# Kernel optimization log

Hardware: AMD Instinct MI355X
Metric: run time of the kernel (lower is better)

Reference implementation:

```python
import jax, jax.numpy as jnp
import numpy as np

NUM_HEADS = 12
HEAD_DIM = 32
GP_NUM = 20


def setup_inputs() -> dict:
    key = jax.random.key(0)
    k1, k2, k3, k4 = jax.random.split(key, 4)
    B, H, W, C = 4, 32, 32, 384
    att = NUM_HEADS * HEAD_DIM  # == C (required by single group_mode)
    x = jax.random.normal(k1, (B, H, W, C), dtype=jnp.float32)
    W_qkv = jax.random.normal(k2, (3 * att, C), dtype=jnp.float32) * (C ** -0.5)
    W_proj = jax.random.normal(k3, (C, att), dtype=jnp.float32) * (att ** -0.5)
    W_gp = jax.random.normal(k4, (GP_NUM, C), dtype=jnp.float32) * (C ** -0.5)
    return {"x": x, "W_qkv": W_qkv, "W_proj": W_proj, "W_gp": W_gp}


def reference(x, W_qkv, W_proj, W_gp):
    B, H, W_, C = x.shape
    N = H * W_
    h, d = NUM_HEADS, HEAD_DIM
    scale = d ** -0.5

    qkv = x.reshape(B, N, C) @ W_qkv.T                      # [B,N,3hd]
    q, k, v = jnp.split(qkv, 3, axis=-1)
    q = q.reshape(B, N, h, d).transpose(0, 2, 1, 3)          # [B,h,N,d]
    k = k.reshape(B, N, h, d).transpose(0, 2, 1, 3)
    v = v.reshape(B, N, h, d).transpose(0, 2, 1, 3)

    attn = jax.nn.softmax(jnp.einsum('bhnd,bhmd->bhnm', q, k) * scale, axis=-1)

    # single group mode: hard top-1 group assignment from all-head q
    q_all = q.transpose(0, 2, 1, 3).reshape(B, N, h * d)     # [B,N,hd]
    gw = q_all @ W_gp.T                                      # [B,N,GP_NUM]
    oh = jax.nn.one_hot(jnp.argmax(gw, axis=-1), GP_NUM, dtype=attn.dtype)
    G = jnp.einsum('bng,bmg->bnm', oh, oh)                   # [B,N,N] same-group mask
    Gh = jnp.concatenate([
        jnp.broadcast_to(G[:, None], (B, h // 2, N, N)),
        jnp.broadcast_to(1.0 - G[:, None], (B, h // 2, N, N)),
    ], axis=1)                                               # [B,h,N,N]

    attn = attn * Gh
    # unusual column-wise renorm: sum over query axis (dim=2)
    attn = attn / (attn.sum(axis=2, keepdims=True) + 1e-8)

    out = jnp.einsum('bhnm,bhmd->bhnd', attn, v)
    out = out.transpose(0, 2, 1, 3).reshape(B, H, W_, h * d)
    return out @ W_proj.T
```

## Files before the change

### kernel.cpp

```cpp
#include <hip/hip_runtime.h>
#include <hip/hip_bf16.h>


#define B_    4
#define N_    1024
#define C_    384
#define H3_   1152
#define NH_   12
#define HD_   32
#define GP_   20
#define BH_   48
#define SCALE 0.17677669529663687f

typedef __attribute__((ext_vector_type(8))) short bf16x8;
typedef __attribute__((ext_vector_type(4))) float f32x4;

static __device__ __forceinline__ unsigned short f2bf(float x) {
  union { float f; unsigned u; } v; v.f = x;
  unsigned r = v.u + 0x7fff + ((v.u >> 16) & 1);
  return (unsigned short)(r >> 16);
}
static __device__ __forceinline__ float bf2f(unsigned short h) {
  union { unsigned u; float f; } v; v.u = ((unsigned)h) << 16;
  return v.f;
}

__global__ __launch_bounds__(256) void conv3(const float* __restrict__ x,
                                             const float* __restrict__ wq,
                                             const float* __restrict__ wp,
                                             unsigned short* __restrict__ xh,
                                             unsigned short* __restrict__ xl,
                                             unsigned short* __restrict__ wqh,
                                             unsigned short* __restrict__ wql,
                                             unsigned short* __restrict__ wph,
                                             unsigned short* __restrict__ wpl) {
  const int NX = (4096 * C_) / 4, NQ = (H3_ * C_) / 4, NP = (C_ * C_) / 4;
  int idx = blockIdx.x * 256 + threadIdx.x;
  const float* src; unsigned short *dh, *dl; int o;
  if (idx < NX)            { src = x;  dh = xh;  dl = xl;  o = idx; }
  else if (idx < NX + NQ)  { src = wq; dh = wqh; dl = wql; o = idx - NX; }
  else if (idx < NX + NQ + NP) { src = wp; dh = wph; dl = wpl; o = idx - NX - NQ; }
  else return;
  float4 v = *(const float4*)(src + (size_t)o * 4);
  float a[4] = {v.x, v.y, v.z, v.w};
  unsigned short h[4], lo[4];
  #pragma unroll
  for (int i = 0; i < 4; ++i) { h[i] = f2bf(a[i]); lo[i] = f2bf(a[i] - bf2f(h[i])); }
  uint2 ph = {(unsigned)h[0]  | ((unsigned)h[1]  << 16),
              (unsigned)h[2]  | ((unsigned)h[3]  << 16)};
  uint2 pl = {(unsigned)lo[0] | ((unsigned)lo[1] << 16),
              (unsigned)lo[2] | ((unsigned)lo[3] << 16)};
  *(uint2*)(dh + (size_t)o * 4) = ph;
  *(uint2*)(dl + (size_t)o * 4) = pl;
}

__global__ __launch_bounds__(256) void wgp_fuse(const float* __restrict__ Wqkv,
                                                const float* __restrict__ Wgp,
                                                double* __restrict__ M) {
  int idx = blockIdx.x * 256 + threadIdx.x;
  if (idx >= GP_ * C_) return;
  int g = idx / C_, c = idx % C_;
  double acc = 0.0;
  for (int j = 0; j < C_; ++j)
    acc += (double)Wgp[g * C_ + j] * (double)Wqkv[(size_t)j * C_ + c];
  M[idx] = acc;
}

__global__ __launch_bounds__(320) void group_assign2(const float* __restrict__ x,
                                                     const double* __restrict__ M,
                                                     int* __restrict__ group) {
  __shared__ double sc[16][GP_];
  int tid = threadIdx.x;
  int r = tid / GP_, g = tid % GP_;
  int n = blockIdx.x * 16 + r;
  const float* row = x + (size_t)n * C_;
  const double* w = M + (size_t)g * C_;
  double acc = 0.0;
  for (int c = 0; c < C_; ++c) acc += (double)row[c] * w[c];
  sc[r][g] = acc;
  __syncthreads();
  if (g == 0) {
    int best = 0; double bv = sc[r][0];
    #pragma unroll
    for (int j = 1; j < GP_; ++j)
      if (sc[r][j] > bv) { bv = sc[r][j]; best = j; }
    group[n] = best;
  }
}

__global__ __launch_bounds__(256) void gemm_qkv(
    const unsigned short* __restrict__ Ah_g, const unsigned short* __restrict__ Al_g,
    const unsigned short* __restrict__ Bh_g, const unsigned short* __restrict__ Bl_g,
    unsigned short* __restrict__ Qh, unsigned short* __restrict__ Ql,
    unsigned short* __restrict__ Kh, unsigned short* __restrict__ Kl,
    float* __restrict__ Vf) {
  __shared__ __align__(16) unsigned short sAh[2][128 * 32];
  __shared__ __align__(16) unsigned short sAl[2][128 * 32];
  __shared__ __align__(16) unsigned short sBh[2][64 * 32];
  __shared__ __align__(16) unsigned short sBl[2][64 * 32];
  int tid = threadIdx.x;
  int l = tid & 63, w = tid >> 6;
  int lanelo = l & 15, g16 = l >> 4;
  int wr = w >> 1, wc = w & 1;
  int flat = blockIdx.x;
  int swz = (flat & 7) * 72 + (flat >> 3);
  int bm = swz / 18, bn = swz % 18;

  int ra = tid >> 2, c4 = tid & 3;
  const unsigned short* gAh0 = Ah_g + (size_t)(bm * 128 + ra) * C_ + c4 * 8;
  const unsigned short* gAl0 = Al_g + (size_t)(bm * 128 + ra) * C_ + c4 * 8;
  const unsigned short* gBh0 = Bh_g + (size_t)(bn * 64 + ra) * C_ + c4 * 8;
  const unsigned short* gBl0 = Bl_g + (size_t)(bn * 64 + ra) * C_ + c4 * 8;
  int dsa = ra * 32 + ((c4 ^ (ra & 3)) * 8);

  uint4 r0 = *(const uint4*)(gAh0);
  uint4 r1 = *(const uint4*)(gAh0 + (size_t)64 * C_);
  uint4 r2 = *(const uint4*)(gAl0);
  uint4 r3 = *(const uint4*)(gAl0 + (size_t)64 * C_);
  uint4 r4 = *(const uint4*)(gBh0);
  uint4 r5 = *(const uint4*)(gBl0);

  f32x4 acc[4][2];
  #pragma unroll
  for (int i = 0; i < 4; ++i)
    #pragma unroll
    for (int j = 0; j < 2; ++j) acc[i][j] = (f32x4){0.f, 0.f, 0.f, 0.f};

  int p = 0;
  for (int kk = 0; kk < 12; ++kk) {
    *(uint4*)(&sAh[p][dsa])           = r0;
    *(uint4*)(&sAh[p][dsa + 64 * 32]) = r1;
    *(uint4*)(&sAl[p][dsa])           = r2;
    *(uint4*)(&sAl[p][dsa + 64 * 32]) = r3;
    *(uint4*)(&sBh[p][dsa])           = r4;
    *(uint4*)(&sBl[p][dsa])           = r5;
    __syncthreads();
    if (kk < 11) {
      int ko = (kk + 1) * 32;
      r0 = *(const uint4*)(gAh0 + ko);
      r1 = *(const uint4*)(gAh0 + (size_t)64 * C_ + ko);
      r2 = *(const uint4*)(gAl0 + ko);
      r3 = *(const uint4*)(gAl0 + (size_t)64 * C_ + ko);
      r4 = *(const uint4*)(gBh0 + ko);
      r5 = *(const uint4*)(gBl0 + ko);
    }
    bf16x8 ah[4], al[4], bh8[2], bl8[2];
    #pragma unroll
    for (int i = 0; i < 4; ++i) {
      int row = wr * 64 + i * 16 + lanelo;
      int off = row * 32 + ((g16 ^ (row & 3)) * 8);
      ah[i] = *(const bf16x8*)(&sAh[p][off]);
      al[i] = *(const bf16x8*)(&sAl[p][off]);
    }
    #pragma unroll
    for (int j = 0; j < 2; ++j) {
      int row = wc * 32 + j * 16 + lanelo;
      int off = row * 32 + ((g16 ^ (row & 3)) * 8);
      bh8[j] = *(const bf16x8*)(&sBh[p][off]);
      bl8[j] = *(const bf16x8*)(&sBl[p][off]);
    }
    #pragma unroll
    for (int i = 0; i < 4; ++i)
      #pragma unroll
      for (int j = 0; j < 2; ++j) {
        acc[i][j] = __builtin_amdgcn_mfma_f32_16x16x32_bf16(ah[i], bh8[j], acc[i][j], 0, 0, 0);
        acc[i][j] = __builtin_amdgcn_mfma_f32_16x16x32_bf16(ah[i], bl8[j], acc[i][j], 0, 0, 0);
        acc[i][j] = __builtin_amdgcn_mfma_f32_16x16x32_bf16(al[i], bh8[j], acc[i][j], 0, 0, 0);
      }
    p ^= 1;
  }

  int region = bn / 6;
  #pragma unroll
  for (int i = 0; i < 4; ++i) {
    int mm0 = bm * 128 + wr * 64 + i * 16 + g16 * 4;
    #pragma unroll
    for (int j = 0; j < 2; ++j) {
      int c = bn * 64 + wc * 32 + j * 16 + lanelo;
      int cc = c - region * 384;
      #pragma unroll
      for (int t = 0; t < 4; ++t) {
        int mm = mm0 + t;
        int b = mm >> 10, n = mm & 1023;
        float v = acc[i][j][t];
        if (region == 0) {
          v *= SCALE;
          unsigned short h = f2bf(v), lo = f2bf(v - bf2f(h));
          size_t idx = ((size_t)(b * NH_ + (cc >> 5)) * N_ + n) * HD_ + (cc & 31);
          Qh[idx] = h; Ql[idx] = lo;
        } else if (region == 1) {
          unsigned short h = f2bf(v), lo = f2bf(v - bf2f(h));
          size_t idx = ((size_t)(b * NH_ + (cc >> 5)) * N_ + n) * HD_ + (cc & 31);
          Kh[idx] = h; Kl[idx] = lo;
        } else {
          Vf[(size_t)mm * C_ + cc] = v;
        }
      }
    }
  }
}

__global__ __launch_bounds__(256) void gemm_proj(
    const unsigned short* __restrict__ Ah_g, const unsigned short* __restrict__ Al_g,
    const unsigned short* __restrict__ Bh_g, const unsigned short* __restrict__ Bl_g,
    float* __restrict__ Cm) {
  __shared__ __align__(16) unsigned short sAh[2][64 * 32];
  __shared__ __align__(16) unsigned short sAl[2][64 * 32];
  __shared__ __align__(16) unsigned short sBh[2][64 * 32];
  __shared__ __align__(16) unsigned short sBl[2][64 * 32];
  int tid = threadIdx.x;
  int l = tid & 63, w = tid >> 6;
  int lanelo = l & 15, g16 = l >> 4;
  int wr = w >> 1, wc = w & 1;
  int flat = blockIdx.x;
  int swz = (flat & 7) * 48 + (flat >> 3);
  int bm = swz / 6, bn = swz % 6;

  int ra = tid >> 2, c4 = tid & 3;
  const unsigned short* gAh0 = Ah_g + (size_t)(bm * 64 + ra) * C_ + c4 * 8;
  const unsigned short* gAl0 = Al_g + (size_t)(bm * 64 + ra) * C_ + c4 * 8;
  const unsigned short* gBh0 = Bh_g + (size_t)(bn * 64 + ra) * C_ + c4 * 8;
  const unsigned short* gBl0 = Bl_g + (size_t)(bn * 64 + ra) * C_ + c4 * 8;
  int dsa = ra * 32 + ((c4 ^ (ra & 3)) * 8);

  uint4 r0 = *(const uint4*)(gAh0);
  uint4 r1 = *(const uint4*)(gAl0);
  uint4 r2 = *(const uint4*)(gBh0);
  uint4 r3 = *(const uint4*)(gBl0);

  f32x4 acc[2][2];
  #pragma unroll
  for (int i = 0; i < 2; ++i)
    #pragma unroll
    for (int j = 0; j < 2; ++j) acc[i][j] = (f32x4){0.f, 0.f, 0.f, 0.f};

  int p = 0;
  for (int kk = 0; kk < 12; ++kk) {
    *(uint4*)(&sAh[p][dsa]) = r0;
    *(uint4*)(&sAl[p][dsa]) = r1;
    *(uint4*)(&sBh[p][dsa]) = r2;
    *(uint4*)(&sBl[p][dsa]) = r3;
    __syncthreads();
    if (kk < 11) {
      int ko = (kk + 1) * 32;
      r0 = *(const uint4*)(gAh0 + ko);
      r1 = *(const uint4*)(gAl0 + ko);
      r2 = *(const uint4*)(gBh0 + ko);
      r3 = *(const uint4*)(gBl0 + ko);
    }
    bf16x8 ah[2], al[2], bh8[2], bl8[2];
    #pragma unroll
    for (int i = 0; i < 2; ++i) {
      int row = wr * 32 + i * 16 + lanelo;
      int off = row * 32 + ((g16 ^ (row & 3)) * 8);
      ah[i] = *(const bf16x8*)(&sAh[p][off]);
      al[i] = *(const bf16x8*)(&sAl[p][off]);
    }
    #pragma unroll
    for (int j = 0; j < 2; ++j) {
      int row = wc * 32 + j * 16 + lanelo;
      int off = row * 32 + ((g16 ^ (row & 3)) * 8);
      bh8[j] = *(const bf16x8*)(&sBh[p][off]);
      bl8[j] = *(const bf16x8*)(&sBl[p][off]);
    }
    #pragma unroll
    for (int i = 0; i < 2; ++i)
      #pragma unroll
      for (int j = 0; j < 2; ++j) {
        acc[i][j] = __builtin_amdgcn_mfma_f32_16x16x32_bf16(ah[i], bh8[j], acc[i][j], 0, 0, 0);
        acc[i][j] = __builtin_amdgcn_mfma_f32_16x16x32_bf16(ah[i], bl8[j], acc[i][j], 0, 0, 0);
        acc[i][j] = __builtin_amdgcn_mfma_f32_16x16x32_bf16(al[i], bh8[j], acc[i][j], 0, 0, 0);
      }
    p ^= 1;
  }
  #pragma unroll
  for (int i = 0; i < 2; ++i) {
    int mm = bm * 64 + wr * 32 + i * 16 + g16 * 4;
    #pragma unroll
    for (int j = 0; j < 2; ++j) {
      int c = bn * 64 + wc * 32 + j * 16 + lanelo;
      #pragma unroll
      for (int t = 0; t < 4; ++t)
        Cm[(size_t)(mm + t) * C_ + c] = acc[i][j][t];
    }
  }
}

__global__ __launch_bounds__(256) void score3(const unsigned short* __restrict__ Qh,
                                              const unsigned short* __restrict__ Ql,
                                              const unsigned short* __restrict__ Kh,
                                              const unsigned short* __restrict__ Kl,
                                              const int* __restrict__ group,
                                              float* __restrict__ rinv,
                                              float* __restrict__ colpart) {
  __shared__ __align__(16) unsigned short kbufh[4096];
  __shared__ __align__(16) unsigned short kbufl[4096];
  __shared__ float colpart_s[4][1024];
  __shared__ int g_s[1024];
  int tid = threadIdx.x;
  int l = tid & 63, w = tid >> 6;
  int lanelo = l & 15, g16 = l >> 4;
  int flat = blockIdx.y * 16 + blockIdx.x;
  int nf = (flat & 7) * 96 + (flat >> 3);
  int bh = nf >> 4, blk = nf & 15;
  int b = bh / NH_;
  bool samehead = ((bh % NH_) < NH_ / 2);
  int q0 = blk * 64 + w * 16;
  size_t bhb = (size_t)bh * (N_ * HD_);

  *(int4*)&g_s[tid * 4] = *(const int4*)(group + b * N_ + tid * 4);
  bf16x8 aQh = *(const bf16x8*)(Qh + bhb + (size_t)(q0 + lanelo) * HD_ + g16 * 8);
  bf16x8 aQl = *(const bf16x8*)(Ql + bhb + (size_t)(q0 + lanelo) * HD_ + g16 * 8);
  __syncthreads();
  int gq[4];
  #pragma unroll
  for (int t = 0; t < 4; ++t) gq[t] = g_s[q0 + g16 * 4 + t];

  float s4[4] = {0.f, 0.f, 0.f, 0.f};
  for (int ch = 0; ch < 8; ++ch) {
    __syncthreads();
    #pragma unroll
    for (int t2 = 0; t2 < 2; ++t2) {
      int f2 = t2 * 256 + tid;
      int row = f2 >> 2, c4 = f2 & 3;
      uint4 vh = *(const uint4*)(Kh + bhb + (size_t)(ch * 128 + row) * HD_ + c4 * 8);
      uint4 vl = *(const uint4*)(Kl + bhb + (size_t)(ch * 128 + row) * HD_ + c4 * 8);
      int phys = row * 64 + ((c4 ^ (row & 3)) << 4);
      *(uint4*)((char*)kbufh + phys) = vh;
      *(uint4*)((char*)kbufl + phys) = vl;
    }
    __syncthreads();
    #pragma unroll
    for (int kt2 = 0; kt2 < 8; ++kt2) {
      int kvl = kt2 * 16 + lanelo;
      int phys = kvl * 64 + ((g16 ^ (kvl & 3)) << 4);
      bf16x8 bh8 = *(const bf16x8*)((char*)kbufh + phys);
      bf16x8 bl8 = *(const bf16x8*)((char*)kbufl + phys);
      f32x4 acc = {0.f, 0.f, 0.f, 0.f};
      acc = __builtin_amdgcn_mfma_f32_16x16x32_bf16(aQh, bh8, acc, 0, 0, 0);
      acc = __builtin_amdgcn_mfma_f32_16x16x32_bf16(aQh, bl8, acc, 0, 0, 0);
      acc = __builtin_amdgcn_mfma_f32_16x16x32_bf16(aQl, bh8, acc, 0, 0, 0);
      #pragma unroll
      for (int t = 0; t < 4; ++t) s4[t] += __expf(acc[t]);
    }
  }
  float ri[4];
  #pragma unroll
  for (int t = 0; t < 4; ++t) {
    #pragma unroll
    for (int off = 1; off < 16; off <<= 1) s4[t] += __shfl_xor(s4[t], off);
    ri[t] = 1.0f / s4[t];
  }
  if (lanelo == 0) {
    #pragma unroll
    for (int t = 0; t < 4; ++t)
      rinv[(size_t)bh * N_ + q0 + g16 * 4 + t] = ri[t];
  }

  for (int ch = 0; ch < 8; ++ch) {
    __syncthreads();
    #pragma unroll
    for (int t2 = 0; t2 < 2; ++t2) {
      int f2 = t2 * 256 + tid;
      int row = f2 >> 2, c4 = f2 & 3;
      uint4 vh = *(const uint4*)(Kh + bhb + (size_t)(ch * 128 + row) * HD_ + c4 * 8);
      uint4 vl = *(const uint4*)(Kl + bhb + (size_t)(ch * 128 + row) * HD_ + c4 * 8);
      int phys = row * 64 + ((c4 ^ (row & 3)) << 4);
      *(uint4*)((char*)kbufh + phys) = vh;
      *(uint4*)((char*)kbufl + phys) = vl;
    }
    __syncthreads();
    #pragma unroll
    for (int kt2 = 0; kt2 < 8; ++kt2) {
      int kt = ch * 8 + kt2;
      int kvl = kt2 * 16 + lanelo;
      int phys = kvl * 64 + ((g16 ^ (kvl & 3)) << 4);
      bf16x8 bh8 = *(const bf16x8*)((char*)kbufh + phys);
      bf16x8 bl8 = *(const bf16x8*)((char*)kbufl + phys);
      f32x4 acc = {0.f, 0.f, 0.f, 0.f};
      acc = __builtin_amdgcn_mfma_f32_16x16x32_bf16(aQh, bh8, acc, 0, 0, 0);
      acc = __builtin_amdgcn_mfma_f32_16x16x32_bf16(aQh, bl8, acc, 0, 0, 0);
      acc = __builtin_amdgcn_mfma_f32_16x16x32_bf16(aQl, bh8, acc, 0, 0, 0);
      int gcol = g_s[kt * 16 + lanelo];
      float cs = 0.f;
      #pragma unroll
      for (int t = 0; t < 4; ++t) {
        bool keep = ((gcol == gq[t]) == samehead);
        cs += keep ? __expf(acc[t]) * ri[t] : 0.f;
      }
      cs += __shfl_xor(cs, 16);
      cs += __shfl_xor(cs, 32);
      if (l < 16) colpart_s[w][kt * 16 + l] = cs;
    }
  }
  __syncthreads();
  int c0 = tid * 4;
  float4 p0 = *(float4*)&colpart_s[0][c0];
  float4 p1 = *(float4*)&colpart_s[1][c0];
  float4 p2 = *(float4*)&colpart_s[2][c0];
  float4 p3 = *(float4*)&colpart_s[3][c0];
  float4 rr = {p0.x + p1.x + p2.x + p3.x, p0.y + p1.y + p2.y + p3.y,
               p0.z + p1.z + p2.z + p3.z, p0.w + p1.w + p2.w + p3.w};
  *(float4*)(colpart + ((size_t)(bh * 16 + blk)) * 1024 + c0) = rr;
}

__global__ __launch_bounds__(256) void vsplit(const float* __restrict__ colpart,
                                              const float* __restrict__ Vf,
                                              unsigned short* __restrict__ Vth,
                                              unsigned short* __restrict__ Vtl) {
  __shared__ float red[256];
  __shared__ float colinv_s[16];
  __shared__ unsigned short vh_s[32][16];
  __shared__ unsigned short vl_s[32][16];
  int tid = threadIdx.x;
  int flat = blockIdx.y * 64 + blockIdx.x;
  int nf = (flat & 7) * 384 + (flat >> 3);
  int bh = nf >> 6, mt = nf & 63;
  int b = bh / NH_, hd = bh % NH_;

  int p = tid >> 4, m16 = tid & 15;
  red[tid] = colpart[((size_t)(bh * 16 + p)) * 1024 + mt * 16 + m16];
  __syncthreads();
  #pragma unroll
  for (int st = 128; st >= 16; st >>= 1) {
    if (tid < st) red[tid] += red[tid + st];
    __syncthreads();
  }
  if (tid < 16) colinv_s[tid] = 1.0f / (red[tid] + 1e-8f);
  __syncthreads();
  if (tid < 128) {
    int m = tid >> 3, d4 = (tid & 7) * 4;
    float4 v = *(const float4*)(Vf + ((size_t)(b * N_ + mt * 16 + m)) * C_ +
                                hd * HD_ + d4);
    float ci = colinv_s[m];
    float va[4] = {v.x * ci, v.y * ci, v.z * ci, v.w * ci};
    #pragma unroll
    for (int i = 0; i < 4; ++i) {
      unsigned short h = f2bf(va[i]);
      vh_s[d4 + i][m] = h;
      vl_s[d4 + i][m] = f2bf(va[i] - bf2f(h));
    }
  }
  __syncthreads();
  if (tid < 64) {
    int d = tid >> 1, m8 = (tid & 1) * 8;
    uint4 h = *(uint4*)&vh_s[d][m8];
    *(uint4*)(Vth + ((size_t)bh * HD_ + d) * N_ + mt * 16 + m8) = h;
  } else if (tid < 128) {
    int t2 = tid - 64;
    int d = t2 >> 1, m8 = (t2 & 1) * 8;
    uint4 lo = *(uint4*)&vl_s[d][m8];
    *(uint4*)(Vtl + ((size_t)bh * HD_ + d) * N_ + mt * 16 + m8) = lo;
  }
}

__global__ __launch_bounds__(256) void pv3(const unsigned short* __restrict__ Qh,
                                           const unsigned short* __restrict__ Ql,
                                           const unsigned short* __restrict__ Kh,
                                           const unsigned short* __restrict__ Kl,
                                           const unsigned short* __restrict__ Vth,
                                           const unsigned short* __restrict__ Vtl,
                                           const int* __restrict__ group,
                                           const float* __restrict__ rinv,
                                           unsigned short* __restrict__ aoh,
                                           unsigned short* __restrict__ aol) {
  __shared__ __align__(16) unsigned short kbufh[4096];
  __shared__ __align__(16) unsigned short kbufl[4096];
  __shared__ __align__(16) unsigned short vbufh[4096];
  __shared__ __align__(16) unsigned short vbufl[4096];
  __shared__ __align__(16) float bounce[4][512];
  __shared__ int g_s[1024];
  int tid = threadIdx.x;
  int l = tid & 63, w = tid >> 6;
  int lanelo = l & 15, g16 = l >> 4;
  int flat = blockIdx.y * 16 + blockIdx.x;
  int nf = (flat & 7) * 96 + (flat >> 3);
  int bh = nf >> 4, blk = nf & 15;
  int b = bh / NH_, hd = bh % NH_;
  bool samehead = (hd < NH_ / 2);
  int q0 = blk * 64 + w * 16;
  size_t bhb = (size_t)bh * (N_ * HD_);

  *(int4*)&g_s[tid * 4] = *(const int4*)(group + b * N_ + tid * 4);
  bf16x8 aQh = *(const bf16x8*)(Qh + bhb + (size_t)(q0 + lanelo) * HD_ + g16 * 8);
  bf16x8 aQl = *(const bf16x8*)(Ql + bhb + (size_t)(q0 + lanelo) * HD_ + g16 * 8);
  float ri[4];
  #pragma unroll
  for (int t = 0; t < 4; ++t)
    ri[t] = rinv[(size_t)bh * N_ + q0 + g16 * 4 + t];
  __syncthreads();
  int gq[4];
  #pragma unroll
  for (int t = 0; t < 4; ++t) gq[t] = g_s[q0 + g16 * 4 + t];

  f32x4 o0 = {0.f, 0.f, 0.f, 0.f};
  f32x4 o1 = {0.f, 0.f, 0.f, 0.f};

  for (int ch = 0; ch < 8; ++ch) {
    __syncthreads();
    #pragma unroll
    for (int t2 = 0; t2 < 2; ++t2) {
      int f2 = t2 * 256 + tid;
      int row = f2 >> 2, c4 = f2 & 3;
      uint4 vh = *(const uint4*)(Kh + bhb + (size_t)(ch * 128 + row) * HD_ + c4 * 8);
      uint4 vl = *(const uint4*)(Kl + bhb + (size_t)(ch * 128 + row) * HD_ + c4 * 8);
      int phys = row * 64 + ((c4 ^ (row & 3)) << 4);
      *(uint4*)((char*)kbufh + phys) = vh;
      *(uint4*)((char*)kbufl + phys) = vl;
    }
    #pragma unroll
    for (int t2 = 0; t2 < 2; ++t2) {
      int f2 = t2 * 256 + tid;
      int d = f2 >> 4, c = f2 & 15;
      uint4 vh = *(const uint4*)(Vth + bhb + (size_t)d * N_ + ch * 128 + c * 8);
      uint4 vl = *(const uint4*)(Vtl + bhb + (size_t)d * N_ + ch * 128 + c * 8);
      int physc = c ^ (d & 15);
      *(uint4*)(vbufh + d * 128 + physc * 8) = vh;
      *(uint4*)(vbufl + d * 128 + physc * 8) = vl;
    }
    __syncthreads();

    #pragma unroll
    for (int pair = 0; pair < 4; ++pair) {
      f32x4 sa[2];
      #pragma unroll
      for (int half = 0; half < 2; ++half) {
        int kvl = pair * 32 + half * 16 + lanelo;
        int phys = kvl * 64 + ((g16 ^ (kvl & 3)) << 4);
        bf16x8 bh8 = *(const bf16x8*)((char*)kbufh + phys);
        bf16x8 bl8 = *(const bf16x8*)((char*)kbufl + phys);
        f32x4 acc = {0.f, 0.f, 0.f, 0.f};
        acc = __builtin_amdgcn_mfma_f32_16x16x32_bf16(aQh, bh8, acc, 0, 0, 0);
        acc = __builtin_amdgcn_mfma_f32_16x16x32_bf16(aQh, bl8, acc, 0, 0, 0);
        acc = __builtin_amdgcn_mfma_f32_16x16x32_bf16(aQl, bh8, acc, 0, 0, 0);
        sa[half] = acc;
      }
      #pragma unroll
      for (int half = 0; half < 2; ++half) {
        int kvloc = pair * 32 + half * 16 + lanelo;
        int gcol = g_s[ch * 128 + kvloc];
        int kv = half * 16 + lanelo;
        int chunk = kv >> 2;
        #pragma unroll
        for (int t = 0; t < 4; ++t) {
          bool keep = ((gcol == gq[t]) == samehead);
          float p = keep ? __expf(sa[half][t]) : 0.f;
          int q = g16 * 4 + t;
          bounce[w][q * 32 + ((chunk ^ (q & 7)) << 2) + (kv & 3)] = p;
        }
      }
      float pf[8];
      int q2 = lanelo;
      int c0i = (2 * g16) ^ (q2 & 7), c1i = (2 * g16 + 1) ^ (q2 & 7);
      *(float4*)&pf[0] = *(float4*)&bounce[w][q2 * 32 + c0i * 4];
      *(float4*)&pf[4] = *(float4*)&bounce[w][q2 * 32 + c1i * 4];
      bf16x8 pa;
      #pragma unroll
      for (int j = 0; j < 8; ++j) pa[j] = (short)f2bf(pf[j]);
      int vchunk = pair * 4 + g16;
      int d0 = lanelo, d1 = 16 + lanelo;
      bf16x8 v0h = *(const bf16x8*)(vbufh + d0 * 128 + ((vchunk ^ (d0 & 15)) << 3));
      bf16x8 v0l = *(const bf16x8*)(vbufl + d0 * 128 + ((vchunk ^ (d0 & 15)) << 3));
      bf16x8 v1h = *(const bf16x8*)(vbufh + d1 * 128 + ((vchunk ^ (d1 & 15)) << 3));
      bf16x8 v1l = *(const bf16x8*)(vbufl + d1 * 128 + ((vchunk ^ (d1 & 15)) << 3));
      o0 = __builtin_amdgcn_mfma_f32_16x16x32_bf16(pa, v0h, o0, 0, 0, 0);
      o0 = __builtin_amdgcn_mfma_f32_16x16x32_bf16(pa, v0l, o0, 0, 0, 0);
      o1 = __builtin_amdgcn_mfma_f32_16x16x32_bf16(pa, v1h, o1, 0, 0, 0);
      o1 = __builtin_amdgcn_mfma_f32_16x16x32_bf16(pa, v1l, o1, 0, 0, 0);
    }
  }
  #pragma unroll
  for (int t = 0; t < 4; ++t) {
    size_t row = (size_t)(b * N_ + q0 + g16 * 4 + t) * C_ + hd * HD_;
    float v0 = o0[t] * ri[t], v1 = o1[t] * ri[t];
    unsigned short h;
    h = f2bf(v0); aoh[row + lanelo]      = h; aol[row + lanelo]      = f2bf(v0 - bf2f(h));
    h = f2bf(v1); aoh[row + 16 + lanelo] = h; aol[row + 16 + lanelo] = f2bf(v1 - bf2f(h));
  }
}

extern "C" void kernel_launch(void* const* d_in, const int* in_sizes, int n_in,
                              void* d_out, int out_size, void* d_ws, size_t ws_size,
                              hipStream_t stream) {
  const float* x     = (const float*)d_in[0];
  const float* Wqkv  = (const float*)d_in[1];
  const float* Wproj = (const float*)d_in[2];
  const float* Wgp   = (const float*)d_in[3];
  float* out = (float*)d_out;

  char* base = (char*)d_ws;
  size_t off = 0;
  auto alloc = [&](size_t bytes) {
    void* p = base + off;
    off += (bytes + 255) & ~(size_t)255;
    return p;
  };
  float*  Vf      = (float*)alloc(4096ull * C_ * 4);
  float*  rinv    = (float*)alloc((size_t)BH_ * N_ * 4);
  float*  colpart = (float*)alloc((size_t)BH_ * 16 * N_ * 4);
  double* Mgp     = (double*)alloc((size_t)GP_ * C_ * 8);
  int*    group   = (int*)alloc(4096ull * 4);
  unsigned short* xh  = (unsigned short*)alloc(4096ull * C_ * 2);
  unsigned short* xl  = (unsigned short*)alloc(4096ull * C_ * 2);
  unsigned short* Wqh = (unsigned short*)alloc((size_t)H3_ * C_ * 2);
  unsigned short* Wql = (unsigned short*)alloc((size_t)H3_ * C_ * 2);
  unsigned short* Wph = (unsigned short*)alloc((size_t)C_ * C_ * 2);
  unsigned short* Wpl = (unsigned short*)alloc((size_t)C_ * C_ * 2);
  unsigned short* aoh = (unsigned short*)alloc(4096ull * C_ * 2);
  unsigned short* aol = (unsigned short*)alloc(4096ull * C_ * 2);
  const size_t BSZ = (size_t)BH_ * N_ * HD_;
  unsigned short* Qh  = (unsigned short*)alloc(BSZ * 2);
  unsigned short* Ql  = (unsigned short*)alloc(BSZ * 2);
  unsigned short* Kh  = (unsigned short*)alloc(BSZ * 2);
  unsigned short* Kl  = (unsigned short*)alloc(BSZ * 2);
  unsigned short* Vth = (unsigned short*)alloc(BSZ * 2);
  unsigned short* Vtl = (unsigned short*)alloc(BSZ * 2);

  conv3<<<dim3(2112), 256, 0, stream>>>(x, Wqkv, Wproj, xh, xl, Wqh, Wql, Wph, Wpl);
  wgp_fuse<<<dim3(30), 256, 0, stream>>>(Wqkv, Wgp, Mgp);
  group_assign2<<<dim3(256), 320, 0, stream>>>(x, Mgp, group);
  gemm_qkv<<<dim3(576), 256, 0, stream>>>(xh, xl, Wqh, Wql,
                                          Qh, Ql, Kh, Kl, Vf);
  score3<<<dim3(16, BH_), 256, 0, stream>>>(Qh, Ql, Kh, Kl, group, rinv, colpart);
  vsplit<<<dim3(64, BH_), 256, 0, stream>>>(colpart, Vf, Vth, Vtl);
  pv3<<<dim3(16, BH_), 256, 0, stream>>>(Qh, Ql, Kh, Kl, Vth, Vtl, group,
                                         rinv, aoh, aol);
  gemm_proj<<<dim3(384), 256, 0, stream>>>(aoh, aol, Wph, Wpl, out);
}
```

Measured before the change: 167.2 us.

## Materialize masked exp scores to global memory instead of recomputing QK in three passes

The score kernel now computes QK^T once. It writes the masked, unnormalized exp values as bf16 into a large global buffer E, tiled as 16 key columns by 1024 queries per block, and accumulates row sums in the same pass. This replaces the previous two-pass score kernel and the QK recomputation in the PV kernel. The Q scale now folds in log2(e) so exp2f can be used. A new colv kernel reduces the column sums from E weighted by rinv. pv5 reads E directly as the MFMA A operand, processes 128 queries per block, and prefetches V into registers. This trades repeated split-precision MFMA work for about 100 MB of extra global memory traffic and bf16 rounding of the probabilities.

```diff
diff --git a/kernel.cpp b/kernel.cpp
--- a/kernel.cpp
+++ b/kernel.cpp
@@ -10,7 +10,7 @@
 #define HD_   32
 #define GP_   20
 #define BH_   48
-#define SCALE 0.17677669529663687f
+#define QSCALE 0.2550029971791444f
 
 typedef __attribute__((ext_vector_type(8))) short bf16x8;
 typedef __attribute__((ext_vector_type(4))) float f32x4;
@@ -184,7 +184,7 @@
         int b = mm >> 10, n = mm & 1023;
         float v = acc[i][j][t];
         if (region == 0) {
-          v *= SCALE;
+          v *= QSCALE;
           unsigned short h = f2bf(v), lo = f2bf(v - bf2f(h));
           size_t idx = ((size_t)(b * NH_ + (cc >> 5)) * N_ + n) * HD_ + (cc & 31);
           Qh[idx] = h; Ql[idx] = lo;
@@ -286,16 +286,16 @@
   }
 }
 
-__global__ __launch_bounds__(256) void score3(const unsigned short* __restrict__ Qh,
+__global__ __launch_bounds__(256) void score5(const unsigned short* __restrict__ Qh,
                                               const unsigned short* __restrict__ Ql,
                                               const unsigned short* __restrict__ Kh,
                                               const unsigned short* __restrict__ Kl,
                                               const int* __restrict__ group,
                                               float* __restrict__ rinv,
-                                              float* __restrict__ colpart) {
+                                              unsigned short* __restrict__ E) {
   __shared__ __align__(16) unsigned short kbufh[4096];
   __shared__ __align__(16) unsigned short kbufl[4096];
-  __shared__ float colpart_s[4][1024];
+  __shared__ __align__(16) float bounce[4][256];
   __shared__ int g_s[1024];
   int tid = threadIdx.x;
   int l = tid & 63, w = tid >> 6;
@@ -317,45 +317,7 @@
   for (int t = 0; t < 4; ++t) gq[t] = g_s[q0 + g16 * 4 + t];
 
   float s4[4] = {0.f, 0.f, 0.f, 0.f};
-  for (int ch = 0; ch < 8; ++ch) {
-    __syncthreads();
-    #pragma unroll
-    for (int t2 = 0; t2 < 2; ++t2) {
-      int f2 = t2 * 256 + tid;
-      int row = f2 >> 2, c4 = f2 & 3;
-      uint4 vh = *(const uint4*)(Kh + bhb + (size_t)(ch * 128 + row) * HD_ + c4 * 8);
-      uint4 vl = *(const uint4*)(Kl + bhb + (size_t)(ch * 128 + row) * HD_ + c4 * 8);
-      int phys = row * 64 + ((c4 ^ (row & 3)) << 4);
-      *(uint4*)((char*)kbufh + phys) = vh;
-      *(uint4*)((char*)kbufl + phys) = vl;
-    }
-    __syncthreads();
-    #pragma unroll
-    for (int kt2 = 0; kt2 < 8; ++kt2) {
-      int kvl = kt2 * 16 + lanelo;
-      int phys = kvl * 64 + ((g16 ^ (kvl & 3)) << 4);
-      bf16x8 bh8 = *(const bf16x8*)((char*)kbufh + phys);
-      bf16x8 bl8 = *(const bf16x8*)((char*)kbufl + phys);
-      f32x4 acc = {0.f, 0.f, 0.f, 0.f};
-      acc = __builtin_amdgcn_mfma_f32_16x16x32_bf16(aQh, bh8, acc, 0, 0, 0);
-      acc = __builtin_amdgcn_mfma_f32_16x16x32_bf16(aQh, bl8, acc, 0, 0, 0);
-      acc = __builtin_amdgcn_mfma_f32_16x16x32_bf16(aQl, bh8, acc, 0, 0, 0);
-      #pragma unroll
-      for (int t = 0; t < 4; ++t) s4[t] += __expf(acc[t]);
-    }
-  }
-  float ri[4];
-  #pragma unroll
-  for (int t = 0; t < 4; ++t) {
-    #pragma unroll
-    for (int off = 1; off < 16; off <<= 1) s4[t] += __shfl_xor(s4[t], off);
-    ri[t] = 1.0f / s4[t];
-  }
-  if (lanelo == 0) {
-    #pragma unroll
-    for (int t = 0; t < 4; ++t)
-      rinv[(size_t)bh * N_ + q0 + g16 * 4 + t] = ri[t];
-  }
+  size_t Eb = (size_t)bh * 64 * 1024 * 16;
 
   for (int ch = 0; ch < 8; ++ch) {
     __syncthreads();
@@ -382,51 +344,82 @@
       acc = __builtin_amdgcn_mfma_f32_16x16x32_bf16(aQh, bl8, acc, 0, 0, 0);
       acc = __builtin_amdgcn_mfma_f32_16x16x32_bf16(aQl, bh8, acc, 0, 0, 0);
       int gcol = g_s[kt * 16 + lanelo];
-      float cs = 0.f;
       #pragma unroll
       for (int t = 0; t < 4; ++t) {
+        float e = exp2f(acc[t]);
+        s4[t] += e;
+        int r = g16 * 4 + t;
         bool keep = ((gcol == gq[t]) == samehead);
-        cs += keep ? __expf(acc[t]) * ri[t] : 0.f;
+        float me = keep ? e : 0.f;
+        int pc = (lanelo >> 2) ^ (r & 3) ^ (r >> 2);
+        bounce[w][r * 16 + pc * 4 + (lanelo & 3)] = me;
       }
-      cs += __shfl_xor(cs, 16);
-      cs += __shfl_xor(cs, 32);
-      if (l < 16) colpart_s[w][kt * 16 + l] = cs;
-    }
-  }
-  __syncthreads();
-  int c0 = tid * 4;
-  float4 p0 = *(float4*)&colpart_s[0][c0];
-  float4 p1 = *(float4*)&colpart_s[1][c0];
-  float4 p2 = *(float4*)&colpart_s[2][c0];
-  float4 p3 = *(float4*)&colpart_s[3][c0];
-  float4 rr = {p0.x + p1.x + p2.x + p3.x, p0.y + p1.y + p2.y + p3.y,
-               p0.z + p1.z + p2.z + p3.z, p0.w + p1.w + p2.w + p3.w};
-  *(float4*)(colpart + ((size_t)(bh * 16 + blk)) * 1024 + c0) = rr;
-}
-
-__global__ __launch_bounds__(256) void vsplit(const float* __restrict__ colpart,
-                                              const float* __restrict__ Vf,
-                                              unsigned short* __restrict__ Vth,
-                                              unsigned short* __restrict__ Vtl) {
-  __shared__ float red[256];
+      int r2 = l >> 2;
+      int pc2 = (l & 3) ^ (r2 & 3) ^ (r2 >> 2);
+      float4 pv4 = *(float4*)&bounce[w][r2 * 16 + pc2 * 4];
+      unsigned u0 = ((unsigned)f2bf(pv4.y) << 16) | f2bf(pv4.x);
+      unsigned u1 = ((unsigned)f2bf(pv4.w) << 16) | f2bf(pv4.z);
+      uint2 st = {u0, u1};
+      *(uint2*)(E + Eb + ((size_t)kt * 1024 + q0 + r2) * 16 + (l & 3) * 4) = st;
+    }
+  }
+  #pragma unroll
+  for (int t = 0; t < 4; ++t) {
+    #pragma unroll
+    for (int off = 1; off < 16; off <<= 1) s4[t] += __shfl_xor(s4[t], off);
+  }
+  if (lanelo == 0) {
+    #pragma unroll
+    for (int t = 0; t < 4; ++t)
+      rinv[(size_t)bh * N_ + q0 + g16 * 4 + t] = 1.0f / s4[t];
+  }
+}
+
+__global__ __launch_bounds__(256) void colv(const unsigned short* __restrict__ E,
+                                            const float* __restrict__ rinv,
+                                            const float* __restrict__ Vf,
+                                            unsigned short* __restrict__ Vth,
+                                            unsigned short* __restrict__ Vtl) {
+  __shared__ float wsum[4][16];
   __shared__ float colinv_s[16];
   __shared__ unsigned short vh_s[32][16];
   __shared__ unsigned short vl_s[32][16];
   int tid = threadIdx.x;
+  int l = tid & 63, w = tid >> 6;
   int flat = blockIdx.y * 64 + blockIdx.x;
   int nf = (flat & 7) * 384 + (flat >> 3);
   int bh = nf >> 6, mt = nf & 63;
   int b = bh / NH_, hd = bh % NH_;
-
-  int p = tid >> 4, m16 = tid & 15;
-  red[tid] = colpart[((size_t)(bh * 16 + p)) * 1024 + mt * 16 + m16];
+  const unsigned short* Eb = E + ((size_t)(bh * 64 + mt)) * 1024 * 16;
+  const float* rv = rinv + (size_t)bh * N_;
+
+  float s[16] = {};
+  #pragma unroll
+  for (int p = 0; p < 4; ++p) {
+    int n = p * 256 + tid;
+    uint4 a = *(const uint4*)(Eb + (size_t)n * 16);
+    uint4 c = *(const uint4*)(Eb + (size_t)n * 16 + 8);
+    float rn = rv[n];
+    unsigned ua[8] = {a.x, a.y, a.z, a.w, c.x, c.y, c.z, c.w};
+    #pragma unroll
+    for (int i = 0; i < 8; ++i) {
+      s[2 * i]     += bf2f((unsigned short)(ua[i] & 0xffff)) * rn;
+      s[2 * i + 1] += bf2f((unsigned short)(ua[i] >> 16)) * rn;
+    }
+  }
+  #pragma unroll
+  for (int i = 0; i < 16; ++i) {
+    #pragma unroll
+    for (int off = 1; off < 64; off <<= 1) s[i] += __shfl_xor(s[i], off);
+  }
+  if (l == 0) {
+    #pragma unroll
+    for (int i = 0; i < 16; ++i) wsum[w][i] = s[i];
+  }
   __syncthreads();
-  #pragma unroll
-  for (int st = 128; st >= 16; st >>= 1) {
-    if (tid < st) red[tid] += red[tid + st];
-    __syncthreads();
-  }
-  if (tid < 16) colinv_s[tid] = 1.0f / (red[tid] + 1e-8f);
+  if (tid < 16)
+    colinv_s[tid] = 1.0f / (wsum[0][tid] + wsum[1][tid] + wsum[2][tid] +
+                            wsum[3][tid] + 1e-8f);
   __syncthreads();
   if (tid < 128) {
     int m = tid >> 3, d4 = (tid & 7) * 4;
@@ -454,128 +447,92 @@
   }
 }
 
-__global__ __launch_bounds__(256) void pv3(const unsigned short* __restrict__ Qh,
-                                           const unsigned short* __restrict__ Ql,
-                                           const unsigned short* __restrict__ Kh,
-                                           const unsigned short* __restrict__ Kl,
+__global__ __launch_bounds__(256) void pv5(const unsigned short* __restrict__ E,
                                            const unsigned short* __restrict__ Vth,
                                            const unsigned short* __restrict__ Vtl,
-                                           const int* __restrict__ group,
                                            const float* __restrict__ rinv,
                                            unsigned short* __restrict__ aoh,
                                            unsigned short* __restrict__ aol) {
-  __shared__ __align__(16) unsigned short kbufh[4096];
-  __shared__ __align__(16) unsigned short kbufl[4096];
   __shared__ __align__(16) unsigned short vbufh[4096];
   __shared__ __align__(16) unsigned short vbufl[4096];
-  __shared__ __align__(16) float bounce[4][512];
-  __shared__ int g_s[1024];
   int tid = threadIdx.x;
   int l = tid & 63, w = tid >> 6;
   int lanelo = l & 15, g16 = l >> 4;
-  int flat = blockIdx.y * 16 + blockIdx.x;
-  int nf = (flat & 7) * 96 + (flat >> 3);
-  int bh = nf >> 4, blk = nf & 15;
+  int flat = blockIdx.y * 8 + blockIdx.x;
+  int nf = (flat & 7) * 48 + (flat >> 3);
+  int bh = nf >> 3, blk = nf & 7;
   int b = bh / NH_, hd = bh % NH_;
-  bool samehead = (hd < NH_ / 2);
-  int q0 = blk * 64 + w * 16;
+  int q0 = blk * 128 + w * 32;
   size_t bhb = (size_t)bh * (N_ * HD_);
-
-  *(int4*)&g_s[tid * 4] = *(const int4*)(group + b * N_ + tid * 4);
-  bf16x8 aQh = *(const bf16x8*)(Qh + bhb + (size_t)(q0 + lanelo) * HD_ + g16 * 8);
-  bf16x8 aQl = *(const bf16x8*)(Ql + bhb + (size_t)(q0 + lanelo) * HD_ + g16 * 8);
-  float ri[4];
-  #pragma unroll
-  for (int t = 0; t < 4; ++t)
-    ri[t] = rinv[(size_t)bh * N_ + q0 + g16 * 4 + t];
-  __syncthreads();
-  int gq[4];
-  #pragma unroll
-  for (int t = 0; t < 4; ++t) gq[t] = g_s[q0 + g16 * 4 + t];
-
-  f32x4 o0 = {0.f, 0.f, 0.f, 0.f};
-  f32x4 o1 = {0.f, 0.f, 0.f, 0.f};
+  size_t Eb = (size_t)bh * 64 * 1024 * 16;
+
+  float ri[2][4];
+  #pragma unroll
+  for (int f = 0; f < 2; ++f)
+    #pragma unroll
+    for (int t = 0; t < 4; ++t)
+      ri[f][t] = rinv[(size_t)bh * N_ + q0 + f * 16 + g16 * 4 + t];
+
+  int vd0 = tid >> 4, vc0 = tid & 15;
+  int vd1 = (256 + tid) >> 4;
+  const unsigned short* vh0 = Vth + bhb + (size_t)vd0 * N_ + vc0 * 8;
+  const unsigned short* vl0 = Vtl + bhb + (size_t)vd0 * N_ + vc0 * 8;
+  const unsigned short* vh1 = Vth + bhb + (size_t)vd1 * N_ + vc0 * 8;
+  const unsigned short* vl1 = Vtl + bhb + (size_t)vd1 * N_ + vc0 * 8;
+  int vp0 = vd0 * 128 + (vc0 ^ (vd0 & 15)) * 8;
+  int vp1 = vd1 * 128 + (vc0 ^ (vd1 & 15)) * 8;
+
+  uint4 vrh0 = *(const uint4*)(vh0), vrh1 = *(const uint4*)(vh1);
+  uint4 vrl0 = *(const uint4*)(vl0), vrl1 = *(const uint4*)(vl1);
+
+  f32x4 o00 = {0.f,0.f,0.f,0.f}, o01 = {0.f,0.f,0.f,0.f};
+  f32x4 o10 = {0.f,0.f,0.f,0.f}, o11 = {0.f,0.f,0.f,0.f};
 
   for (int ch = 0; ch < 8; ++ch) {
+    if (ch) __syncthreads();
+    *(uint4*)(vbufh + vp0) = vrh0;
+    *(uint4*)(vbufh + vp1) = vrh1;
+    *(uint4*)(vbufl + vp0) = vrl0;
+    *(uint4*)(vbufl + vp1) = vrl1;
     __syncthreads();
-    #pragma unroll
-    for (int t2 = 0; t2 < 2; ++t2) {
-      int f2 = t2 * 256 + tid;
-      int row = f2 >> 2, c4 = f2 & 3;
-      uint4 vh = *(const uint4*)(Kh + bhb + (size_t)(ch * 128 + row) * HD_ + c4 * 8);
-      uint4 vl = *(const uint4*)(Kl + bhb + (size_t)(ch * 128 + row) * HD_ + c4 * 8);
-      int phys = row * 64 + ((c4 ^ (row & 3)) << 4);
-      *(uint4*)((char*)kbufh + phys) = vh;
-      *(uint4*)((char*)kbufl + phys) = vl;
-    }
-    #pragma unroll
-    for (int t2 = 0; t2 < 2; ++t2) {
-      int f2 = t2 * 256 + tid;
-      int d = f2 >> 4, c = f2 & 15;
-      uint4 vh = *(const uint4*)(Vth + bhb + (size_t)d * N_ + ch * 128 + c * 8);
-      uint4 vl = *(const uint4*)(Vtl + bhb + (size_t)d * N_ + ch * 128 + c * 8);
-      int physc = c ^ (d & 15);
-      *(uint4*)(vbufh + d * 128 + physc * 8) = vh;
-      *(uint4*)(vbufl + d * 128 + physc * 8) = vl;
-    }
-    __syncthreads();
-
+    if (ch < 7) {
+      int vko = (ch + 1) * 128;
+      vrh0 = *(const uint4*)(vh0 + vko); vrh1 = *(const uint4*)(vh1 + vko);
+      vrl0 = *(const uint4*)(vl0 + vko); vrl1 = *(const uint4*)(vl1 + vko);
+    }
     #pragma unroll
     for (int pair = 0; pair < 4; ++pair) {
-      f32x4 sa[2];
-      #pragma unroll
-      for (int half = 0; half < 2; ++half) {
-        int kvl = pair * 32 + half * 16 + lanelo;
-        int phys = kvl * 64 + ((g16 ^ (kvl & 3)) << 4);
-        bf16x8 bh8 = *(const bf16x8*)((char*)kbufh + phys);
-        bf16x8 bl8 = *(const bf16x8*)((char*)kbufl + phys);
-        f32x4 acc = {0.f, 0.f, 0.f, 0.f};
-        acc = __builtin_amdgcn_mfma_f32_16x16x32_bf16(aQh, bh8, acc, 0, 0, 0);
-        acc = __builtin_amdgcn_mfma_f32_16x16x32_bf16(aQh, bl8, acc, 0, 0, 0);
-        acc = __builtin_amdgcn_mfma_f32_16x16x32_bf16(aQl, bh8, acc, 0, 0, 0);
-        sa[half] = acc;
-      }
-      #pragma unroll
-      for (int half = 0; half < 2; ++half) {
-        int kvloc = pair * 32 + half * 16 + lanelo;
-        int gcol = g_s[ch * 128 + kvloc];
-        int kv = half * 16 + lanelo;
-        int chunk = kv >> 2;
-        #pragma unroll
-        for (int t = 0; t < 4; ++t) {
-          bool keep = ((gcol == gq[t]) == samehead);
-          float p = keep ? __expf(sa[half][t]) : 0.f;
-          int q = g16 * 4 + t;
-          bounce[w][q * 32 + ((chunk ^ (q & 7)) << 2) + (kv & 3)] = p;
-        }
-      }
-      float pf[8];
-      int q2 = lanelo;
-      int c0i = (2 * g16) ^ (q2 & 7), c1i = (2 * g16 + 1) ^ (q2 & 7);
-      *(float4*)&pf[0] = *(float4*)&bounce[w][q2 * 32 + c0i * 4];
-      *(float4*)&pf[4] = *(float4*)&bounce[w][q2 * 32 + c1i * 4];
-      bf16x8 pa;
-      #pragma unroll
-      for (int j = 0; j < 8; ++j) pa[j] = (short)f2bf(pf[j]);
+      int kt = ch * 8 + pair * 2 + (g16 >> 1);
+      int mi = (g16 & 1) * 8;
+      bf16x8 a0 = *(const bf16x8*)(E + Eb + ((size_t)kt * 1024 + q0 + lanelo) * 16 + mi);
+      bf16x8 a1 = *(const bf16x8*)(E + Eb + ((size_t)kt * 1024 + q0 + 16 + lanelo) * 16 + mi);
       int vchunk = pair * 4 + g16;
       int d0 = lanelo, d1 = 16 + lanelo;
       bf16x8 v0h = *(const bf16x8*)(vbufh + d0 * 128 + ((vchunk ^ (d0 & 15)) << 3));
       bf16x8 v0l = *(const bf16x8*)(vbufl + d0 * 128 + ((vchunk ^ (d0 & 15)) << 3));
       bf16x8 v1h = *(const bf16x8*)(vbufh + d1 * 128 + ((vchunk ^ (d1 & 15)) << 3));
       bf16x8 v1l = *(const bf16x8*)(vbufl + d1 * 128 + ((vchunk ^ (d1 & 15)) << 3));
-      o0 = __builtin_amdgcn_mfma_f32_16x16x32_bf16(pa, v0h, o0, 0, 0, 0);
-      o0 = __builtin_amdgcn_mfma_f32_16x16x32_bf16(pa, v0l, o0, 0, 0, 0);
-      o1 = __builtin_amdgcn_mfma_f32_16x16x32_bf16(pa, v1h, o1, 0, 0, 0);
-      o1 = __builtin_amdgcn_mfma_f32_16x16x32_bf16(pa, v1l, o1, 0, 0, 0);
+      o00 = __builtin_amdgcn_mfma_f32_16x16x32_bf16(a0, v0h, o00, 0, 0, 0);
+      o00 = __builtin_amdgcn_mfma_f32_16x16x32_bf16(a0, v0l, o00, 0, 0, 0);
+      o01 = __builtin_amdgcn_mfma_f32_16x16x32_bf16(a0, v1h, o01, 0, 0, 0);
+      o01 = __builtin_amdgcn_mfma_f32_16x16x32_bf16(a0, v1l, o01, 0, 0, 0);
+      o10 = __builtin_amdgcn_mfma_f32_16x16x32_bf16(a1, v0h, o10, 0, 0, 0);
+      o10 = __builtin_amdgcn_mfma_f32_16x16x32_bf16(a1, v0l, o10, 0, 0, 0);
+      o11 = __builtin_amdgcn_mfma_f32_16x16x32_bf16(a1, v1h, o11, 0, 0, 0);
+      o11 = __builtin_amdgcn_mfma_f32_16x16x32_bf16(a1, v1l, o11, 0, 0, 0);
     }
   }
   #pragma unroll
   for (int t = 0; t < 4; ++t) {
-    size_t row = (size_t)(b * N_ + q0 + g16 * 4 + t) * C_ + hd * HD_;
-    float v0 = o0[t] * ri[t], v1 = o1[t] * ri[t];
+    size_t row0 = (size_t)(b * N_ + q0 + g16 * 4 + t) * C_ + hd * HD_;
+    size_t row1 = (size_t)(b * N_ + q0 + 16 + g16 * 4 + t) * C_ + hd * HD_;
+    float v00 = o00[t] * ri[0][t], v01 = o01[t] * ri[0][t];
+    float v10 = o10[t] * ri[1][t], v11 = o11[t] * ri[1][t];
     unsigned short h;
-    h = f2bf(v0); aoh[row + lanelo]      = h; aol[row + lanelo]      = f2bf(v0 - bf2f(h));
-    h = f2bf(v1); aoh[row + 16 + lanelo] = h; aol[row + 16 + lanelo] = f2bf(v1 - bf2f(h));
+    h = f2bf(v00); aoh[row0 + lanelo]      = h; aol[row0 + lanelo]      = f2bf(v00 - bf2f(h));
+    h = f2bf(v01); aoh[row0 + 16 + lanelo] = h; aol[row0 + 16 + lanelo] = f2bf(v01 - bf2f(h));
+    h = f2bf(v10); aoh[row1 + lanelo]      = h; aol[row1 + lanelo]      = f2bf(v10 - bf2f(h));
+    h = f2bf(v11); aoh[row1 + 16 + lanelo] = h; aol[row1 + 16 + lanelo] = f2bf(v11 - bf2f(h));
   }
 }
 
@@ -597,7 +554,6 @@
   };
   float*  Vf      = (float*)alloc(4096ull * C_ * 4);
   float*  rinv    = (float*)alloc((size_t)BH_ * N_ * 4);
-  float*  colpart = (float*)alloc((size_t)BH_ * 16 * N_ * 4);
   double* Mgp     = (double*)alloc((size_t)GP_ * C_ * 8);
   int*    group   = (int*)alloc(4096ull * 4);
   unsigned short* xh  = (unsigned short*)alloc(4096ull * C_ * 2);
@@ -615,15 +571,15 @@
   unsigned short* Kl  = (unsigned short*)alloc(BSZ * 2);
   unsigned short* Vth = (unsigned short*)alloc(BSZ * 2);
   unsigned short* Vtl = (unsigned short*)alloc(BSZ * 2);
+  unsigned short* E   = (unsigned short*)alloc((size_t)BH_ * N_ * N_ * 2);
 
   conv3<<<dim3(2112), 256, 0, stream>>>(x, Wqkv, Wproj, xh, xl, Wqh, Wql, Wph, Wpl);
   wgp_fuse<<<dim3(30), 256, 0, stream>>>(Wqkv, Wgp, Mgp);
   group_assign2<<<dim3(256), 320, 0, stream>>>(x, Mgp, group);
   gemm_qkv<<<dim3(576), 256, 0, stream>>>(xh, xl, Wqh, Wql,
                                           Qh, Ql, Kh, Kl, Vf);
-  score3<<<dim3(16, BH_), 256, 0, stream>>>(Qh, Ql, Kh, Kl, group, rinv, colpart);
-  vsplit<<<dim3(64, BH_), 256, 0, stream>>>(colpart, Vf, Vth, Vtl);
-  pv3<<<dim3(16, BH_), 256, 0, stream>>>(Qh, Ql, Kh, Kl, Vth, Vtl, group,
-                                         rinv, aoh, aol);
+  score5<<<dim3(16, BH_), 256, 0, stream>>>(Qh, Ql, Kh, Kl, group, rinv, E);
+  colv<<<dim3(64, BH_), 256, 0, stream>>>(E, rinv, Vf, Vth, Vtl);
+  pv5<<<dim3(8, BH_), 256, 0, stream>>>(E, Vth, Vtl, rinv, aoh, aol);
   gemm_proj<<<dim3(384), 256, 0, stream>>>(aoh, aol, Wph, Wpl, out);
 }
```

Result: no change. 169.1 us (+1.1%).

## Register-prefetch K/V tiles, fold log2e into Q scale, vectorize group scoring

Applied to the files above, without the earlier changes.

The attention kernels now load the next K (and V) chunk into registers while the MFMA work on the current LDS tile runs, hiding global load latency behind compute. Q is pre-scaled by scale*log2(e) so the exponentials can use exp2f instead of __expf, which removes a multiply per score. The group-assignment dot product is vectorized with float4/double2 loads. The register prefetch raises register pressure, which may cut occupancy.

```diff
diff --git a/kernel.cpp b/kernel.cpp
--- a/kernel.cpp
+++ b/kernel.cpp
@@ -10,7 +10,7 @@
 #define HD_   32
 #define GP_   20
 #define BH_   48
-#define SCALE 0.17677669529663687f
+#define QSCALE 0.2550029971791444f
 
 typedef __attribute__((ext_vector_type(8))) short bf16x8;
 typedef __attribute__((ext_vector_type(4))) float f32x4;
@@ -76,7 +76,14 @@
   const float* row = x + (size_t)n * C_;
   const double* w = M + (size_t)g * C_;
   double acc = 0.0;
-  for (int c = 0; c < C_; ++c) acc += (double)row[c] * w[c];
+  #pragma unroll 4
+  for (int c = 0; c < C_; c += 4) {
+    float4 xv = *(const float4*)(row + c);
+    double2 w0 = *(const double2*)(w + c);
+    double2 w1 = *(const double2*)(w + c + 2);
+    acc += (double)xv.x * w0.x + (double)xv.y * w0.y +
+           (double)xv.z * w1.x + (double)xv.w * w1.y;
+  }
   sc[r][g] = acc;
   __syncthreads();
   if (g == 0) {
@@ -184,7 +191,7 @@
         int b = mm >> 10, n = mm & 1023;
         float v = acc[i][j][t];
         if (region == 0) {
-          v *= SCALE;
+          v *= QSCALE;
           unsigned short h = f2bf(v), lo = f2bf(v - bf2f(h));
           size_t idx = ((size_t)(b * NH_ + (cc >> 5)) * N_ + n) * HD_ + (cc & 31);
           Qh[idx] = h; Ql[idx] = lo;
@@ -316,20 +323,33 @@
   #pragma unroll
   for (int t = 0; t < 4; ++t) gq[t] = g_s[q0 + g16 * 4 + t];
 
+  int srow = tid >> 2, sc4 = tid & 3;
+  const unsigned short* kh0 = Kh + bhb + (size_t)srow * HD_ + sc4 * 8;
+  const unsigned short* kl0 = Kl + bhb + (size_t)srow * HD_ + sc4 * 8;
+  int ph0 = srow * 64 + ((sc4 ^ (srow & 3)) << 4);
+  const int ROWOFF = 64 * HD_;
+  const int PHOFF = 64 * 64;
+
+  uint4 rh0 = *(const uint4*)(kh0);
+  uint4 rh1 = *(const uint4*)(kh0 + ROWOFF);
+  uint4 rl0 = *(const uint4*)(kl0);
+  uint4 rl1 = *(const uint4*)(kl0 + ROWOFF);
+
   float s4[4] = {0.f, 0.f, 0.f, 0.f};
   for (int ch = 0; ch < 8; ++ch) {
+    if (ch) __syncthreads();
+    *(uint4*)((char*)kbufh + ph0)         = rh0;
+    *(uint4*)((char*)kbufh + ph0 + PHOFF) = rh1;
+    *(uint4*)((char*)kbufl + ph0)         = rl0;
+    *(uint4*)((char*)kbufl + ph0 + PHOFF) = rl1;
     __syncthreads();
-    #pragma unroll
-    for (int t2 = 0; t2 < 2; ++t2) {
-      int f2 = t2 * 256 + tid;
-      int row = f2 >> 2, c4 = f2 & 3;
-      uint4 vh = *(const uint4*)(Kh + bhb + (size_t)(ch * 128 + row) * HD_ + c4 * 8);
-      uint4 vl = *(const uint4*)(Kl + bhb + (size_t)(ch * 128 + row) * HD_ + c4 * 8);
-      int phys = row * 64 + ((c4 ^ (row & 3)) << 4);
-      *(uint4*)((char*)kbufh + phys) = vh;
-      *(uint4*)((char*)kbufl + phys) = vl;
-    }
-    __syncthreads();
+    if (ch < 7) {
+      int ko = (ch + 1) * 128 * HD_;
+      rh0 = *(const uint4*)(kh0 + ko);
+      rh1 = *(const uint4*)(kh0 + ko + ROWOFF);
+      rl0 = *(const uint4*)(kl0 + ko);
+      rl1 = *(const uint4*)(kl0 + ko + ROWOFF);
+    }
     #pragma unroll
     for (int kt2 = 0; kt2 < 8; ++kt2) {
       int kvl = kt2 * 16 + lanelo;
@@ -341,9 +361,13 @@
       acc = __builtin_amdgcn_mfma_f32_16x16x32_bf16(aQh, bl8, acc, 0, 0, 0);
       acc = __builtin_amdgcn_mfma_f32_16x16x32_bf16(aQl, bh8, acc, 0, 0, 0);
       #pragma unroll
-      for (int t = 0; t < 4; ++t) s4[t] += __expf(acc[t]);
-    }
-  }
+      for (int t = 0; t < 4; ++t) s4[t] += exp2f(acc[t]);
+    }
+  }
+  rh0 = *(const uint4*)(kh0);
+  rh1 = *(const uint4*)(kh0 + ROWOFF);
+  rl0 = *(const uint4*)(kl0);
+  rl1 = *(const uint4*)(kl0 + ROWOFF);
   float ri[4];
   #pragma unroll
   for (int t = 0; t < 4; ++t) {
@@ -359,17 +383,18 @@
 
   for (int ch = 0; ch < 8; ++ch) {
     __syncthreads();
-    #pragma unroll
-    for (int t2 = 0; t2 < 2; ++t2) {
-      int f2 = t2 * 256 + tid;
-      int row = f2 >> 2, c4 = f2 & 3;
-      uint4 vh = *(const uint4*)(Kh + bhb + (size_t)(ch * 128 + row) * HD_ + c4 * 8);
-      uint4 vl = *(const uint4*)(Kl + bhb + (size_t)(ch * 128 + row) * HD_ + c4 * 8);
-      int phys = row * 64 + ((c4 ^ (row & 3)) << 4);
-      *(uint4*)((char*)kbufh + phys) = vh;
-      *(uint4*)((char*)kbufl + phys) = vl;
-    }
+    *(uint4*)((char*)kbufh + ph0)         = rh0;
+    *(uint4*)((char*)kbufh + ph0 + PHOFF) = rh1;
+    *(uint4*)((char*)kbufl + ph0)         = rl0;
+    *(uint4*)((char*)kbufl + ph0 + PHOFF) = rl1;
     __syncthreads();
+    if (ch < 7) {
+      int ko = (ch + 1) * 128 * HD_;
+      rh0 = *(const uint4*)(kh0 + ko);
+      rh1 = *(const uint4*)(kh0 + ko + ROWOFF);
+      rl0 = *(const uint4*)(kl0 + ko);
+      rl1 = *(const uint4*)(kl0 + ko + ROWOFF);
+    }
     #pragma unroll
     for (int kt2 = 0; kt2 < 8; ++kt2) {
       int kt = ch * 8 + kt2;
@@ -386,7 +411,7 @@
       #pragma unroll
       for (int t = 0; t < 4; ++t) {
         bool keep = ((gcol == gq[t]) == samehead);
-        cs += keep ? __expf(acc[t]) * ri[t] : 0.f;
+        cs += keep ? exp2f(acc[t]) * ri[t] : 0.f;
       }
       cs += __shfl_xor(cs, 16);
       cs += __shfl_xor(cs, 32);
@@ -493,32 +518,54 @@
   #pragma unroll
   for (int t = 0; t < 4; ++t) gq[t] = g_s[q0 + g16 * 4 + t];
 
+  int srow = tid >> 2, sc4 = tid & 3;
+  const unsigned short* kh0 = Kh + bhb + (size_t)srow * HD_ + sc4 * 8;
+  const unsigned short* kl0 = Kl + bhb + (size_t)srow * HD_ + sc4 * 8;
+  int kp0 = srow * 64 + ((sc4 ^ (srow & 3)) << 4);
+  const int KROWOFF = 64 * HD_;
+  const int KPHOFF = 64 * 64;
+  int vd0 = tid >> 4, vc0 = tid & 15;
+  const unsigned short* vh0 = Vth + bhb + (size_t)vd0 * N_ + vc0 * 8;
+  const unsigned short* vl0 = Vtl + bhb + (size_t)vd0 * N_ + vc0 * 8;
+  int vp0 = vd0 * 128 + ((vc0 ^ (vd0 & 15)) * 8);
+  const int VROWOFF = 16 * N_;
+  const int VPOFF = 16 * 128;
+
+  uint4 krh0 = *(const uint4*)(kh0);
+  uint4 krh1 = *(const uint4*)(kh0 + KROWOFF);
+  uint4 krl0 = *(const uint4*)(kl0);
+  uint4 krl1 = *(const uint4*)(kl0 + KROWOFF);
+  uint4 vrh0 = *(const uint4*)(vh0);
+  uint4 vrh1 = *(const uint4*)(vh0 + VROWOFF);
+  uint4 vrl0 = *(const uint4*)(vl0);
+  uint4 vrl1 = *(const uint4*)(vl0 + VROWOFF);
+
   f32x4 o0 = {0.f, 0.f, 0.f, 0.f};
   f32x4 o1 = {0.f, 0.f, 0.f, 0.f};
 
   for (int ch = 0; ch < 8; ++ch) {
+    if (ch) __syncthreads();
+    *(uint4*)((char*)kbufh + kp0)          = krh0;
+    *(uint4*)((char*)kbufh + kp0 + KPHOFF) = krh1;
+    *(uint4*)((char*)kbufl + kp0)          = krl0;
+    *(uint4*)((char*)kbufl + kp0 + KPHOFF) = krl1;
+    *(uint4*)(vbufh + vp0)         = vrh0;
+    *(uint4*)(vbufh + vp0 + VPOFF) = vrh1;
+    *(uint4*)(vbufl + vp0)         = vrl0;
+    *(uint4*)(vbufl + vp0 + VPOFF) = vrl1;
     __syncthreads();
-    #pragma unroll
-    for (int t2 = 0; t2 < 2; ++t2) {
-      int f2 = t2 * 256 + tid;
-      int row = f2 >> 2, c4 = f2 & 3;
-      uint4 vh = *(const uint4*)(Kh + bhb + (size_t)(ch * 128 + row) * HD_ + c4 * 8);
-      uint4 vl = *(const uint4*)(Kl + bhb + (size_t)(ch * 128 + row) * HD_ + c4 * 8);
-      int phys = row * 64 + ((c4 ^ (row & 3)) << 4);
-      *(uint4*)((char*)kbufh + phys) = vh;
-      *(uint4*)((char*)kbufl + phys) = vl;
-    }
-    #pragma unroll
-    for (int t2 = 0; t2 < 2; ++t2) {
-      int f2 = t2 * 256 + tid;
-      int d = f2 >> 4, c = f2 & 15;
-      uint4 vh = *(const uint4*)(Vth + bhb + (size_t)d * N_ + ch * 128 + c * 8);
-      uint4 vl = *(const uint4*)(Vtl + bhb + (size_t)d * N_ + ch * 128 + c * 8);
-      int physc = c ^ (d & 15);
-      *(uint4*)(vbufh + d * 128 + physc * 8) = vh;
-      *(uint4*)(vbufl + d * 128 + physc * 8) = vl;
-    }
-    __syncthreads();
+    if (ch < 7) {
+      int kko = (ch + 1) * 128 * HD_;
+      int vko = (ch + 1) * 128;
+      krh0 = *(const uint4*)(kh0 + kko);
+      krh1 = *(const uint4*)(kh0 + kko + KROWOFF);
+      krl0 = *(const uint4*)(kl0 + kko);
+      krl1 = *(const uint4*)(kl0 + kko + KROWOFF);
+      vrh0 = *(const uint4*)(vh0 + vko);
+      vrh1 = *(const uint4*)(vh0 + vko + VROWOFF);
+      vrl0 = *(const uint4*)(vl0 + vko);
+      vrl1 = *(const uint4*)(vl0 + vko + VROWOFF);
+    }
 
     #pragma unroll
     for (int pair = 0; pair < 4; ++pair) {
@@ -544,7 +591,7 @@
         #pragma unroll
         for (int t = 0; t < 4; ++t) {
           bool keep = ((gcol == gq[t]) == samehead);
-          float p = keep ? __expf(sa[half][t]) : 0.f;
+          float p = keep ? exp2f(sa[half][t]) : 0.f;
           int q = g16 * 4 + t;
           bounce[w][q * 32 + ((chunk ^ (q & 7)) << 2) + (kv & 3)] = p;
         }
```

Result: slower. 175.7 us (+5.1%).
